# Kernel tuning notes

Measured on AMD Instinct MI355X. Metric: run time of the kernel, lower is better.

## Reference

```python
import jax, jax.numpy as jnp
import numpy as np

N = 50000      # nodes
F = 128        # in_channels
H = 4          # heads
C = 32         # out_channels per head
E = 800000     # edges (before self-loops)
NEG_SLOPE = 0.2


def setup_inputs() -> dict:
    key = jax.random.key(0)
    ks = jax.random.split(key, 10)
    x = jax.random.normal(ks[0], (N, F), dtype=jnp.float32)
    edge_index = jax.random.randint(ks[1], (2, E), 0, N, dtype=jnp.int32)
    s = 1.0 / np.sqrt(F)
    Wl = jax.random.uniform(ks[2], (H * C, F), jnp.float32, -s, s)
    bl = jax.random.uniform(ks[3], (H * C,), jnp.float32, -s, s)
    Wr = jax.random.uniform(ks[4], (H * C, F), jnp.float32, -s, s)
    br = jax.random.uniform(ks[5], (H * C,), jnp.float32, -s, s)
    Ws = jax.random.uniform(ks[6], (H * C, F), jnp.float32, -s, s)
    bs = jax.random.uniform(ks[7], (H * C,), jnp.float32, -s, s)
    att = jax.random.normal(ks[8], (H, C), jnp.float32) * (1.0 / np.sqrt(C))
    bias = jnp.zeros((H * C,), jnp.float32)
    return {"x": x, "edge_index": edge_index, "Wl": Wl, "bl": bl,
            "Wr": Wr, "br": br, "Ws": Ws, "bs": bs, "att": att, "bias": bias}


def reference(x, edge_index, Wl, bl, Wr, br, Ws, bs, att, bias):
    # add self loops (add_self_loops=True, edge_dim=None)
    loop = jnp.arange(N, dtype=edge_index.dtype)
    src = jnp.concatenate([edge_index[0], loop])  # j (source / neighbor)
    dst = jnp.concatenate([edge_index[1], loop])  # i (target, softmax segment)

    xl = (x @ Wl.T + bl).reshape(N, H, C)  # attention source transform (lin_l = lin_lAP)
    xr = (x @ Wr.T + br).reshape(N, H, C)  # attention target transform (lin_r = lin_rAP)
    xs = (x @ Ws.T + bs).reshape(N, H, C)  # aggregation transform (lin_s, linAggrSharing=False)

    # GATv2 edge score: a^T LeakyReLU(Theta_l x_j + Theta_r x_i)
    e = jax.nn.leaky_relu(xl[src] + xr[dst], NEG_SLOPE)      # [E+N, H, C]
    score = jnp.einsum('ehc,hc->eh', e, att)                 # [E+N, H]

    # segment softmax over incoming edges of each target node
    m = jax.ops.segment_max(score, dst, num_segments=N)      # [N, H]
    p = jnp.exp(score - m[dst])
    denom = jax.ops.segment_sum(p, dst, num_segments=N)      # [N, H]
    alpha = p / denom[dst]                                   # [E+N, H]

    # weighted scatter-add aggregation of lin_s-transformed sources
    out = jax.ops.segment_sum(xs[src] * alpha[..., None], dst, num_segments=N)
    return out.reshape(N, H * C) + bias                      # concat=True
```

## Files before the change

### kernel.cpp

```cpp
#include <hip/hip_runtime.h>
#include <hip/hip_bf16.h>

#define GN 50000
#define GF 128
#define GH 4
#define GC 32
#define GE 800000
#define GETOT (GE + GN)
#define HC 128
#define NEG 0.2f

typedef __bf16 bf16x8 __attribute__((ext_vector_type(8)));
typedef float  f32x4  __attribute__((ext_vector_type(4)));
typedef unsigned short ushort8 __attribute__((ext_vector_type(8)));

__device__ __forceinline__ ushort f32_to_bf16_rne(float f) {
    unsigned u = __float_as_uint(f);
    return (ushort)((u + 0x7fffu + ((u >> 16) & 1u)) >> 16);
}

__device__ __forceinline__ bf16x8 cvt8(const float* p) {
    float4 v0 = *(const float4*)p;
    float4 v1 = *(const float4*)(p + 4);
    ushort8 o;
    o[0] = f32_to_bf16_rne(v0.x); o[1] = f32_to_bf16_rne(v0.y);
    o[2] = f32_to_bf16_rne(v0.z); o[3] = f32_to_bf16_rne(v0.w);
    o[4] = f32_to_bf16_rne(v1.x); o[5] = f32_to_bf16_rne(v1.y);
    o[6] = f32_to_bf16_rne(v1.z); o[7] = f32_to_bf16_rne(v1.w);
    return __builtin_bit_cast(bf16x8, o);
}

__global__ __launch_bounds__(256) void conv_w(
    const float* __restrict__ Wl, const float* __restrict__ Wr,
    const float* __restrict__ Ws, ushort* __restrict__ Wb)
{
    int idx = blockIdx.x * 256 + threadIdx.x;
    if (idx >= 3 * GF * GF / 8) return;
    int m = idx / 2048;
    int e = (idx - m * 2048) * 8;
    const float* W = (m == 0) ? Wl : (m == 1) ? Wr : Ws;
    float4 v0 = *(const float4*)&W[e];
    float4 v1 = *(const float4*)&W[e + 4];
    ushort8 o;
    o[0] = f32_to_bf16_rne(v0.x); o[1] = f32_to_bf16_rne(v0.y);
    o[2] = f32_to_bf16_rne(v0.z); o[3] = f32_to_bf16_rne(v0.w);
    o[4] = f32_to_bf16_rne(v1.x); o[5] = f32_to_bf16_rne(v1.y);
    o[6] = f32_to_bf16_rne(v1.z); o[7] = f32_to_bf16_rne(v1.w);
    *(ushort8*)&Wb[m * 16384 + e] = o;
}

__global__ __launch_bounds__(256) void transform_mfma(
    const float* __restrict__ x, const ushort* __restrict__ Wb,
    const float* __restrict__ bl, const float* __restrict__ br,
    const float* __restrict__ bs,
    ushort* __restrict__ xi, float* __restrict__ xr)
{
    const int m     = blockIdx.y;
    const int wave  = threadIdx.x >> 6;
    const int lane  = threadIdx.x & 63;
    const int colb  = lane & 15;
    const int klane = lane >> 4;
    const int row0  = blockIdx.x * 128 + wave * 32;

    bf16x8 a[2][4];
#pragma unroll
    for (int s = 0; s < 2; ++s) {
        int rA = row0 + s * 16 + colb;
        const float* ap = x + (size_t)min(rA, GN - 1) * GF + klane * 8;
#pragma unroll
        for (int kb = 0; kb < 4; ++kb)
            a[s][kb] = cvt8(ap + kb * 32);
    }

    const ushort* wb = Wb + m * 16384 + colb * GF + klane * 8;

    f32x4 acc[2][8];
#pragma unroll
    for (int s = 0; s < 2; ++s)
#pragma unroll
        for (int n = 0; n < 8; ++n) acc[s][n] = (f32x4){0.f, 0.f, 0.f, 0.f};

#pragma unroll
    for (int kb = 0; kb < 4; ++kb) {
        bf16x8 b[8];
#pragma unroll
        for (int n = 0; n < 8; ++n)
            b[n] = *(const bf16x8*)(wb + n * 2048 + kb * 32);
#pragma unroll
        for (int n = 0; n < 8; ++n) {
            acc[0][n] = __builtin_amdgcn_mfma_f32_16x16x32_bf16(a[0][kb], b[n], acc[0][n], 0, 0, 0);
            acc[1][n] = __builtin_amdgcn_mfma_f32_16x16x32_bf16(a[1][kb], b[n], acc[1][n], 0, 0, 0);
        }
    }

    const float* bia = (m == 0) ? bl : (m == 1) ? br : bs;
    const int moff = (m == 2) ? 2 : 0;
#pragma unroll
    for (int s = 0; s < 2; ++s) {
        int rD0 = row0 + s * 16 + klane * 4;
#pragma unroll
        for (int n = 0; n < 8; ++n) {
            int col = n * 16 + colb;
            float bv = bia[col];
#pragma unroll
            for (int r = 0; r < 4; ++r) {
                int row = rD0 + r;
                if (row < GN) {
                    float v = acc[s][n][r] + bv;
                    if (m == 1)
                        xr[(size_t)row * HC + col] = v;
                    else
                        xi[(size_t)row * 256 + (col >> 1) * 4 + (col & 1) + moff]
                            = f32_to_bf16_rne(v);
                }
            }
        }
    }
}

__global__ void slot_kernel(const int* __restrict__ ei, int* __restrict__ deg,
                            int* __restrict__ slot)
{
    int e = blockIdx.x * 256 + threadIdx.x;
    if (e >= GETOT) return;
    int dst = (e < GE) ? ei[GE + e] : (e - GE);
    slot[e] = atomicAdd(&deg[dst], 1);
}

__global__ __launch_bounds__(1024) void scan_kernel(const int* __restrict__ deg,
                                                    int* __restrict__ rowstart)
{
    __shared__ int sums[1024];
    const int t = threadIdx.x;
    const int CH = 52;
    const int start = t * CH;
    const int end = min(start + CH, GN);

    int s = 0;
    if (start + CH <= GN) {
#pragma unroll
        for (int g = 0; g < 13; ++g) {
            int4 v = *(const int4*)&deg[start + g * 4];
            s += v.x + v.y + v.z + v.w;
        }
    } else {
        for (int i = start; i < end; ++i) s += deg[i];
    }
    sums[t] = s;
    __syncthreads();
    for (int off = 1; off < 1024; off <<= 1) {
        int v = (t >= off) ? sums[t - off] : 0;
        __syncthreads();
        sums[t] += v;
        __syncthreads();
    }
    int run = sums[t] - s;
    if (start + CH <= GN) {
#pragma unroll
        for (int g = 0; g < 13; ++g) {
            int4 v = *(const int4*)&deg[start + g * 4];
            int4 w;
            w.x = run;
            w.y = run + v.x;
            w.z = run + v.x + v.y;
            w.w = run + v.x + v.y + v.z;
            run += v.x + v.y + v.z + v.w;
            *(int4*)&rowstart[start + g * 4] = w;
        }
    } else {
        for (int i = start; i < end; ++i) { rowstart[i] = run; run += deg[i]; }
    }
    if (t == 1023) rowstart[GN] = run;
}

__global__ void scatter_kernel(const int* __restrict__ ei,
                               const int* __restrict__ rowstart,
                               const int* __restrict__ slot,
                               int* __restrict__ csr_src)
{
    int e = blockIdx.x * 256 + threadIdx.x;
    if (e >= GETOT) return;
    int src, dst;
    if (e < GE) { src = ei[e]; dst = ei[GE + e]; }
    else        { src = dst = e - GE; }
    csr_src[rowstart[dst] + slot[e]] = src;
}

__global__ __launch_bounds__(256) void gat_kernel(
    const ushort* __restrict__ xi, const float* __restrict__ xr,
    const float* __restrict__ att, const float* __restrict__ bias,
    const int* __restrict__ rowstart, const int* __restrict__ csr_src,
    float* __restrict__ out)
{
    const int wave = threadIdx.x >> 6;
    const int lane = threadIdx.x & 63;
    const int node = blockIdx.x * 4 + wave;
    const int l2 = lane * 2;

    const float2 xr2 = *(const float2*)&xr[(size_t)node * HC + l2];
    const float2 at2 = *(const float2*)&att[l2];
    const float2 bi2 = *(const float2*)&bias[l2];

    const int s0 = rowstart[node];
    const int s1 = rowstart[node + 1];

    float denom = 0.f, ax = 0.f, ay = 0.f;
    for (int base = s0; base < s1; base += 64) {
        int nsrc = (base + lane < s1) ? csr_src[base + lane] : 0;
        int cnt = min(64, s1 - base);
        for (int t = 0; t < cnt; ++t) {
            int src = __shfl(nsrc, t, 64);
            uint2 xv = *(const uint2*)&xi[(size_t)src * 256 + l2 * 2];
            float zx = __uint_as_float((xv.x & 0xffffu) << 16) + xr2.x;
            float zy = __uint_as_float(xv.x & 0xffff0000u) + xr2.y;
            zx = (zx > 0.f) ? zx : NEG * zx;
            zy = (zy > 0.f) ? zy : NEG * zy;
            float sc = fmaf(zx, at2.x, zy * at2.y);
            sc += __shfl_xor(sc, 1, 64);
            sc += __shfl_xor(sc, 2, 64);
            sc += __shfl_xor(sc, 4, 64);
            sc += __shfl_xor(sc, 8, 64);
            float pe = __expf(sc);
            denom += pe;
            float sx = __uint_as_float((xv.y & 0xffffu) << 16);
            float sy = __uint_as_float(xv.y & 0xffff0000u);
            ax = fmaf(pe, sx, ax);
            ay = fmaf(pe, sy, ay);
        }
    }
    const float inv = 1.f / denom;
    float2 o;
    o.x = fmaf(ax, inv, bi2.x);
    o.y = fmaf(ay, inv, bi2.y);
    *(float2*)&out[(size_t)node * HC + l2] = o;
}

extern "C" void kernel_launch(void* const* d_in, const int* in_sizes, int n_in,
                              void* d_out, int out_size, void* d_ws, size_t ws_size,
                              hipStream_t stream)
{
    const float* x   = (const float*)d_in[0];
    const int*   ei  = (const int*)  d_in[1];
    const float* Wl  = (const float*)d_in[2];
    const float* bl  = (const float*)d_in[3];
    const float* Wr  = (const float*)d_in[4];
    const float* br  = (const float*)d_in[5];
    const float* Ws  = (const float*)d_in[6];
    const float* bs  = (const float*)d_in[7];
    const float* att = (const float*)d_in[8];
    const float* bias= (const float*)d_in[9];
    float* out = (float*)d_out;

    ushort* xi = (ushort*)d_ws;
    ushort* Wb = xi + (size_t)GN * 256;
    float*  xr = (float*)(Wb + 3 * GF * GF);
    int* deg      = (int*)(xr + (size_t)GN * HC);
    int* rowstart = deg + GN;
    int* slot     = rowstart + GN + 1;
    int* csr_src  = slot + GETOT;

    hipMemsetAsync(deg, 0, GN * sizeof(int), stream);

    conv_w<<<(3 * GF * GF / 8 + 255) / 256, 256, 0, stream>>>(Wl, Wr, Ws, Wb);

    dim3 gt((GN + 127) / 128, 3);
    transform_mfma<<<gt, 256, 0, stream>>>(x, Wb, bl, br, bs, xi, xr);

    int eblocks = (GETOT + 255) / 256;
    slot_kernel<<<eblocks, 256, 0, stream>>>(ei, deg, slot);
    scan_kernel<<<1, 1024, 0, stream>>>(deg, rowstart);
    scatter_kernel<<<eblocks, 256, 0, stream>>>(ei, rowstart, slot, csr_src);

    gat_kernel<<<GN / 4, 256, 0, stream>>>((const ushort*)xi, xr, att, bias,
                                           rowstart, csr_src, out);
}
```

Before: 300.3 us.

## Fuse degree counting into transform launch, fold memset, unroll gather loop by four

The separate memset of the degree array is folded into the weight-conversion kernel. The per-edge slot/atomic-degree kernel is merged with the MFMA projection kernel into one launch, with a flattened grid whose first blocks do edge counting and whose remaining blocks do the three projections. The GAT aggregation loop now loads four neighbor rows at once and masks tail edges by zeroing their weight, which exposes more independent memory loads per wave. The aim is to cut launch and serialization overhead and improve latency hiding in the gather. In exchange, the tail iterations do wasted loads and score work for padded edges.

```diff
diff --git a/kernel.cpp b/kernel.cpp
--- a/kernel.cpp
+++ b/kernel.cpp
@@ -9,6 +9,10 @@
 #define GETOT (GE + GN)
 #define HC 128
 #define NEG 0.2f
+
+#define TBLK 391
+#define TTOT (TBLK * 3)
+#define SBLK ((GETOT + 255) / 256)
 
 typedef __bf16 bf16x8 __attribute__((ext_vector_type(8)));
 typedef float  f32x4  __attribute__((ext_vector_type(4)));
@@ -32,35 +36,52 @@
 
 __global__ __launch_bounds__(256) void conv_w(
     const float* __restrict__ Wl, const float* __restrict__ Wr,
-    const float* __restrict__ Ws, ushort* __restrict__ Wb)
+    const float* __restrict__ Ws, ushort* __restrict__ Wb,
+    int* __restrict__ deg)
 {
     int idx = blockIdx.x * 256 + threadIdx.x;
-    if (idx >= 3 * GF * GF / 8) return;
-    int m = idx / 2048;
-    int e = (idx - m * 2048) * 8;
-    const float* W = (m == 0) ? Wl : (m == 1) ? Wr : Ws;
-    float4 v0 = *(const float4*)&W[e];
-    float4 v1 = *(const float4*)&W[e + 4];
-    ushort8 o;
-    o[0] = f32_to_bf16_rne(v0.x); o[1] = f32_to_bf16_rne(v0.y);
-    o[2] = f32_to_bf16_rne(v0.z); o[3] = f32_to_bf16_rne(v0.w);
-    o[4] = f32_to_bf16_rne(v1.x); o[5] = f32_to_bf16_rne(v1.y);
-    o[6] = f32_to_bf16_rne(v1.z); o[7] = f32_to_bf16_rne(v1.w);
-    *(ushort8*)&Wb[m * 16384 + e] = o;
-}
-
-__global__ __launch_bounds__(256) void transform_mfma(
+    if (idx < 3 * GF * GF / 8) {
+        int m = idx / 2048;
+        int e = (idx - m * 2048) * 8;
+        const float* W = (m == 0) ? Wl : (m == 1) ? Wr : Ws;
+        float4 v0 = *(const float4*)&W[e];
+        float4 v1 = *(const float4*)&W[e + 4];
+        ushort8 o;
+        o[0] = f32_to_bf16_rne(v0.x); o[1] = f32_to_bf16_rne(v0.y);
+        o[2] = f32_to_bf16_rne(v0.z); o[3] = f32_to_bf16_rne(v0.w);
+        o[4] = f32_to_bf16_rne(v1.x); o[5] = f32_to_bf16_rne(v1.y);
+        o[6] = f32_to_bf16_rne(v1.z); o[7] = f32_to_bf16_rne(v1.w);
+        *(ushort8*)&Wb[m * 16384 + e] = o;
+    }
+    int z = idx - 6144;
+    if (z >= 0 && z < GN / 4)
+        *(int4*)&deg[z * 4] = make_int4(0, 0, 0, 0);
+}
+
+__global__ __launch_bounds__(256) void fused_transform_slot(
     const float* __restrict__ x, const ushort* __restrict__ Wb,
     const float* __restrict__ bl, const float* __restrict__ br,
     const float* __restrict__ bs,
+    const int* __restrict__ ei, int* __restrict__ deg, int* __restrict__ slot,
     ushort* __restrict__ xi, float* __restrict__ xr)
 {
-    const int m     = blockIdx.y;
+    if (blockIdx.x < SBLK) {
+        int e = blockIdx.x * 256 + threadIdx.x;
+        if (e < GETOT) {
+            int dst = (e < GE) ? ei[GE + e] : (e - GE);
+            slot[e] = atomicAdd(&deg[dst], 1);
+        }
+        return;
+    }
+
+    const int tb    = blockIdx.x - SBLK;
+    const int m     = tb / TBLK;
+    const int bx    = tb - m * TBLK;
     const int wave  = threadIdx.x >> 6;
     const int lane  = threadIdx.x & 63;
     const int colb  = lane & 15;
     const int klane = lane >> 4;
-    const int row0  = blockIdx.x * 128 + wave * 32;
+    const int row0  = bx * 128 + wave * 32;
 
     bf16x8 a[2][4];
 #pragma unroll
@@ -118,15 +139,6 @@
     }
 }
 
-__global__ void slot_kernel(const int* __restrict__ ei, int* __restrict__ deg,
-                            int* __restrict__ slot)
-{
-    int e = blockIdx.x * 256 + threadIdx.x;
-    if (e >= GETOT) return;
-    int dst = (e < GE) ? ei[GE + e] : (e - GE);
-    slot[e] = atomicAdd(&deg[dst], 1);
-}
-
 __global__ __launch_bounds__(1024) void scan_kernel(const int* __restrict__ deg,
                                                     int* __restrict__ rowstart)
 {
@@ -186,6 +198,25 @@
     csr_src[rowstart[dst] + slot[e]] = src;
 }
 
+__device__ __forceinline__ void edge_acc(uint2 xv, float2 xr2, float2 at2,
+                                         bool live, float& denom,
+                                         float& ax, float& ay)
+{
+    float zx = __uint_as_float((xv.x & 0xffffu) << 16) + xr2.x;
+    float zy = __uint_as_float(xv.x & 0xffff0000u) + xr2.y;
+    zx = (zx > 0.f) ? zx : NEG * zx;
+    zy = (zy > 0.f) ? zy : NEG * zy;
+    float sc = fmaf(zx, at2.x, zy * at2.y);
+    sc += __shfl_xor(sc, 1, 64);
+    sc += __shfl_xor(sc, 2, 64);
+    sc += __shfl_xor(sc, 4, 64);
+    sc += __shfl_xor(sc, 8, 64);
+    float pe = live ? __expf(sc) : 0.f;
+    denom += pe;
+    ax = fmaf(pe, __uint_as_float((xv.y & 0xffffu) << 16), ax);
+    ay = fmaf(pe, __uint_as_float(xv.y & 0xffff0000u), ay);
+}
+
 __global__ __launch_bounds__(256) void gat_kernel(
     const ushort* __restrict__ xi, const float* __restrict__ xr,
     const float* __restrict__ att, const float* __restrict__ bias,
@@ -195,11 +226,11 @@
     const int wave = threadIdx.x >> 6;
     const int lane = threadIdx.x & 63;
     const int node = blockIdx.x * 4 + wave;
-    const int l2 = lane * 2;
-
-    const float2 xr2 = *(const float2*)&xr[(size_t)node * HC + l2];
-    const float2 at2 = *(const float2*)&att[l2];
-    const float2 bi2 = *(const float2*)&bias[l2];
+    const int l4 = lane * 4;
+
+    const float2 xr2 = *(const float2*)&xr[(size_t)node * HC + lane * 2];
+    const float2 at2 = *(const float2*)&att[lane * 2];
+    const float2 bi2 = *(const float2*)&bias[lane * 2];
 
     const int s0 = rowstart[node];
     const int s1 = rowstart[node + 1];
@@ -208,31 +239,26 @@
     for (int base = s0; base < s1; base += 64) {
         int nsrc = (base + lane < s1) ? csr_src[base + lane] : 0;
         int cnt = min(64, s1 - base);
-        for (int t = 0; t < cnt; ++t) {
-            int src = __shfl(nsrc, t, 64);
-            uint2 xv = *(const uint2*)&xi[(size_t)src * 256 + l2 * 2];
-            float zx = __uint_as_float((xv.x & 0xffffu) << 16) + xr2.x;
-            float zy = __uint_as_float(xv.x & 0xffff0000u) + xr2.y;
-            zx = (zx > 0.f) ? zx : NEG * zx;
-            zy = (zy > 0.f) ? zy : NEG * zy;
-            float sc = fmaf(zx, at2.x, zy * at2.y);
-            sc += __shfl_xor(sc, 1, 64);
-            sc += __shfl_xor(sc, 2, 64);
-            sc += __shfl_xor(sc, 4, 64);
-            sc += __shfl_xor(sc, 8, 64);
-            float pe = __expf(sc);
-            denom += pe;
-            float sx = __uint_as_float((xv.y & 0xffffu) << 16);
-            float sy = __uint_as_float(xv.y & 0xffff0000u);
-            ax = fmaf(pe, sx, ax);
-            ay = fmaf(pe, sy, ay);
+        for (int t = 0; t < cnt; t += 4) {
+            int sA = __shfl(nsrc, t, 64);
+            int sB = __shfl(nsrc, t + 1, 64);
+            int sC = __shfl(nsrc, t + 2, 64);
+            int sD = __shfl(nsrc, t + 3, 64);
+            uint2 vA = *(const uint2*)&xi[(size_t)sA * 256 + l4];
+            uint2 vB = *(const uint2*)&xi[(size_t)sB * 256 + l4];
+            uint2 vC = *(const uint2*)&xi[(size_t)sC * 256 + l4];
+            uint2 vD = *(const uint2*)&xi[(size_t)sD * 256 + l4];
+            edge_acc(vA, xr2, at2, true,          denom, ax, ay);
+            edge_acc(vB, xr2, at2, (t + 1 < cnt), denom, ax, ay);
+            edge_acc(vC, xr2, at2, (t + 2 < cnt), denom, ax, ay);
+            edge_acc(vD, xr2, at2, (t + 3 < cnt), denom, ax, ay);
         }
     }
     const float inv = 1.f / denom;
     float2 o;
     o.x = fmaf(ax, inv, bi2.x);
     o.y = fmaf(ay, inv, bi2.y);
-    *(float2*)&out[(size_t)node * HC + l2] = o;
+    *(float2*)&out[(size_t)node * HC + lane * 2] = o;
 }
 
 extern "C" void kernel_launch(void* const* d_in, const int* in_sizes, int n_in,
@@ -259,17 +285,14 @@
     int* slot     = rowstart + GN + 1;
     int* csr_src  = slot + GETOT;
 
-    hipMemsetAsync(deg, 0, GN * sizeof(int), stream);
-
-    conv_w<<<(3 * GF * GF / 8 + 255) / 256, 256, 0, stream>>>(Wl, Wr, Ws, Wb);
-
-    dim3 gt((GN + 127) / 128, 3);
-    transform_mfma<<<gt, 256, 0, stream>>>(x, Wb, bl, br, bs, xi, xr);
-
-    int eblocks = (GETOT + 255) / 256;
-    slot_kernel<<<eblocks, 256, 0, stream>>>(ei, deg, slot);
+    conv_w<<<(6144 + GN / 4 + 255) / 256, 256, 0, stream>>>(Wl, Wr, Ws, Wb, deg);
+
+    fused_transform_slot<<<SBLK + TTOT, 256, 0, stream>>>(
+        x, Wb, bl, br, bs, ei, deg, slot, xi, xr);
+
     scan_kernel<<<1, 1024, 0, stream>>>(deg, rowstart);
-    scatter_kernel<<<eblocks, 256, 0, stream>>>(ei, rowstart, slot, csr_src);
+
+    scatter_kernel<<<SBLK, 256, 0, stream>>>(ei, rowstart, slot, csr_src);
 
     gat_kernel<<<GN / 4, 256, 0, stream>>>((const ushort*)xi, xr, att, bias,
                                            rowstart, csr_src, out);
```

After: 274.3 us. -8.6%, faster.
